# Optimization experiments

Hardware: AMD Instinct MI355X
Metric: run time of the kernel (lower is better)

Reference implementation:

```python
import jax, jax.numpy as jnp
import numpy as np

B, Q, E = 32768, 1024, 1024  # batch, quant_dim, embed_dim


def setup_inputs() -> dict:
    key = jax.random.key(0)
    k1, k2, k3, k4, k5 = jax.random.split(key, 5)
    s = lambda n: 1.0 / np.sqrt(n)
    x = jax.random.normal(k1, (B, Q), jnp.float32)
    # nn.Linear weights, shape [out_features, in_features]
    W1 = jax.random.normal(k2, (2 * Q, Q), jnp.float32) * s(Q)      # selector layer 1
    W2 = jax.random.normal(k3, (Q, 2 * Q), jnp.float32) * s(2 * Q)  # selector layer 2
    W3 = jax.random.normal(k4, (Q, Q), jnp.float32) * s(Q)          # selector layer 3
    Wc = jax.random.normal(k5, (E, Q), jnp.float32) * s(Q)          # codebook
    return {"x": x, "W1": W1, "W2": W2, "W3": W3, "Wc": Wc}


def dyn_k_hot(x, k_scores):
    # k per row = argmax(k_scores) + 1
    k_values = jnp.argmax(k_scores, axis=-1, keepdims=True) + 1  # [B,1]
    # torch: sorted_indices = argsort(x, descending); mask gathered by argsort(sorted_indices)
    # equivalently: rank of each element in descending order < k
    ranks = jnp.argsort(jnp.argsort(-x, axis=-1), axis=-1)       # [B,Q]
    return (ranks < k_values).astype(x.dtype)


def reference(x, W1, W2, W3, Wc):
    # dynkselector: Linear -> ReLU -> Linear -> ReLU -> Linear (no biases)
    h = jax.nn.relu(x @ W1.T)
    h = jax.nn.relu(h @ W2.T)
    k_scores = h @ W3.T
    k_hot = dyn_k_hot(x, k_scores)   # [B,Q] {0,1}
    return k_hot @ Wc.T              # codebook projection -> [B,E]
```

## Files before the change

### kernel.cpp

```cpp
#include <hip/hip_runtime.h>
#include <stdint.h>

#define B_  32768
#define Q_  1024
#define E_  1024
#define CAPF  16384
#define CAPF2 1024

typedef __attribute__((ext_vector_type(8))) short bf16x8;
typedef __attribute__((ext_vector_type(8))) _Float16 f16x8;
typedef __attribute__((ext_vector_type(8))) unsigned short u16x8;
typedef __attribute__((ext_vector_type(4))) float f32x4;
typedef unsigned short us;

__device__ __forceinline__ f32x4 MFMA16(bf16x8 a, bf16x8 b, f32x4 c) {
    return __builtin_amdgcn_mfma_f32_16x16x32_bf16(a, b, c, 0, 0, 0);
}
__device__ __forceinline__ f32x4 MFMA16H(bf16x8 a, bf16x8 b, f32x4 c) {
    return __builtin_amdgcn_mfma_f32_16x16x32_f16(
        __builtin_bit_cast(f16x8, a), __builtin_bit_cast(f16x8, b), c, 0, 0, 0);
}

__device__ __forceinline__ us f2bf(float v) {
    unsigned u = __float_as_uint(v);
    u += 0x7FFFu + ((u >> 16) & 1u);
    return (us)(u >> 16);
}
__device__ __forceinline__ float bf2f(us b) {
    return __uint_as_float(((unsigned)b) << 16);
}
__device__ __forceinline__ us f2h(float v) {
    _Float16 h = (_Float16)v;
    return __builtin_bit_cast(unsigned short, h);
}

__global__ __launch_bounds__(256)
void split_planes_k(const float* __restrict__ in, us* __restrict__ hi,
                    us* __restrict__ lo, int n8) {
    int i = blockIdx.x * 256 + threadIdx.x;
    const int stride = gridDim.x * 256;
    for (; i < n8; i += stride) {
        float4 a = ((const float4*)in)[i * 2];
        float4 b = ((const float4*)in)[i * 2 + 1];
        float f[8] = {a.x, a.y, a.z, a.w, b.x, b.y, b.z, b.w};
        u16x8 h, l;
#pragma unroll
        for (int j = 0; j < 8; ++j) {
            us c0 = f2bf(f[j]);
            h[j] = c0;
            l[j] = f2bf(f[j] - bf2f(c0));
        }
        ((u16x8*)hi)[i] = h;
        ((u16x8*)lo)[i] = l;
    }
}

__global__ __launch_bounds__(256)
void cvt_plane_k(const float* __restrict__ in, us* __restrict__ hi, int n8) {
    int i = blockIdx.x * 256 + threadIdx.x;
    const int stride = gridDim.x * 256;
    for (; i < n8; i += stride) {
        float4 a = ((const float4*)in)[i * 2];
        float4 b = ((const float4*)in)[i * 2 + 1];
        float f[8] = {a.x, a.y, a.z, a.w, b.x, b.y, b.z, b.w};
        u16x8 h;
#pragma unroll
        for (int j = 0; j < 8; ++j) h[j] = f2bf(f[j]);
        ((u16x8*)hi)[i] = h;
    }
}

__global__ __launch_bounds__(256)
void cvt_plane_h(const float* __restrict__ in, us* __restrict__ hi, int n8) {
    int i = blockIdx.x * 256 + threadIdx.x;
    const int stride = gridDim.x * 256;
    for (; i < n8; i += stride) {
        float4 a = ((const float4*)in)[i * 2];
        float4 b = ((const float4*)in)[i * 2 + 1];
        float f[8] = {a.x, a.y, a.z, a.w, b.x, b.y, b.z, b.w};
        u16x8 h;
#pragma unroll
        for (int j = 0; j < 8; ++j) h[j] = f2h(f[j]);
        ((u16x8*)hi)[i] = h;
    }
}

__global__ __launch_bounds__(256)
void gather_split(const float* __restrict__ X, const int* __restrict__ flags,
                  const int* __restrict__ cnt, us* __restrict__ G0,
                  us* __restrict__ G1) {
    const int n = min(*cnt, CAPF);
    for (int it = blockIdx.x; it < n; it += gridDim.x) {
        int row = flags[it];
        if ((unsigned)row >= B_) row = 0;
        float4 v = ((const float4*)(X + (size_t)row * Q_))[threadIdx.x];
        float f[4] = {v.x, v.y, v.z, v.w};
        us h[4], l[4];
#pragma unroll
        for (int j = 0; j < 4; ++j) {
            h[j] = f2bf(f[j]);
            l[j] = f2bf(f[j] - bf2f(h[j]));
        }
        *(uint2*)&G0[(size_t)it * Q_ + threadIdx.x * 4] = *(uint2*)h;
        *(uint2*)&G1[(size_t)it * Q_ + threadIdx.x * 4] = *(uint2*)l;
    }
}

#define LGKM0() asm volatile("s_waitcnt lgkmcnt(0)" ::: "memory")
#define VMC8()  asm volatile("s_waitcnt vmcnt(8)" ::: "memory")
#define BAR()   __builtin_amdgcn_s_barrier()
#define RD_AB(Aarr, Barr, slot) { \
    const us* _la = &LA[(slot) * 8192]; const us* _lb = &LB[(slot) * 8192]; \
    _Pragma("unroll") for (int mf = 0; mf < 8; ++mf) Aarr[mf] = *(const bf16x8*)&_la[ago[mf]]; \
    _Pragma("unroll") for (int nf = 0; nf < 4; ++nf) Barr[nf] = *(const bf16x8*)&_lb[bgo[nf]]; }
#define CLX(AF, BF) { __builtin_amdgcn_s_setprio(1); \
    _Pragma("unroll") for (int mf = 0; mf < 8; ++mf) { \
        _Pragma("unroll") for (int nf = 0; nf < 4; ++nf) { \
            if constexpr (FP16) acc[mf][nf] = MFMA16H(AF[mf], BF[nf], acc[mf][nf]); \
            else               acc[mf][nf] = MFMA16 (AF[mf], BF[nf], acc[mf][nf]); } } \
    __builtin_amdgcn_s_setprio(0); }

template<int NSEG, int K, int EMIT, bool RELU, bool FP16>
__global__ __launch_bounds__(512, 2)
void gemm4r(const us* __restrict__ A0p, const us* __restrict__ A1p,
            const us* __restrict__ B0p, const us* __restrict__ B1p,
            void* __restrict__ Cp0, void* __restrict__ Cp1, int N) {
    constexpr int TPS = K / 32;
    constexpr int NT  = NSEG * TPS;
    static_assert(NT % 2 == 0 && NT >= 4, "shape");
    __shared__ __align__(16) us LA[4 * 8192];
    __shared__ __align__(16) us LB[4 * 8192];

    const int t = threadIdx.x;
    const int wv = t >> 6, lane = t & 63;
    const int lanelo = lane & 15, kq = lane >> 4;
    const int wm = wv >> 2, wn = wv & 3;

    const int q8 = gridDim.x >> 3;
    const int logical = ((int)blockIdx.x & 7) * q8 + ((int)blockIdx.x >> 3);
    const int gx = N >> 8;
    const int m0 = (logical / gx) * 256, n0 = (logical % gx) * 256;

    int soff[2], ldst[2];
#pragma unroll
    for (int i = 0; i < 2; ++i) {
        int s = i * 512 + t;
        int row = s >> 2, c = s & 3;
        soff[i] = row * K + (c ^ ((row >> 1) & 3)) * 8;
        ldst[i] = (i * 512 + wv * 64) * 8;
    }
    int ago[8], bgo[4];
#pragma unroll
    for (int mf = 0; mf < 8; ++mf) {
        int row = wm * 128 + mf * 16 + lanelo;
        ago[mf] = (row * 4 + (kq ^ ((row >> 1) & 3))) * 8;
    }
#pragma unroll
    for (int nf = 0; nf < 4; ++nf) {
        int row = wn * 64 + nf * 16 + lanelo;
        bgo[nf] = (row * 4 + (kq ^ ((row >> 1) & 3))) * 8;
    }

    auto stage = [&](int tv) {
        int slot = tv & 3;
        int seg = tv / TPS;
        int kb  = (tv - seg * TPS) * 32;
        const us* Ap = (NSEG == 1 || seg < 2) ? A0p : A1p;
        const us* Bp = (NSEG == 3 && seg == 1) ? B1p : B0p;
        const us* Abase = Ap + (size_t)m0 * K + kb;
        const us* Bbase = Bp + (size_t)n0 * K + kb;
        us* dA = &LA[slot * 8192];
        us* dB = &LB[slot * 8192];
#pragma unroll
        for (int i = 0; i < 2; ++i) {
            __builtin_amdgcn_global_load_lds(
                (const __attribute__((address_space(1))) void*)(Abase + soff[i]),
                (__attribute__((address_space(3))) void*)(dA + ldst[i]), 16, 0, 0);
            __builtin_amdgcn_global_load_lds(
                (const __attribute__((address_space(1))) void*)(Bbase + soff[i]),
                (__attribute__((address_space(3))) void*)(dB + ldst[i]), 16, 0, 0);
        }
    };

    f32x4 acc[8][4];
#pragma unroll
    for (int i = 0; i < 8; ++i)
#pragma unroll
        for (int j = 0; j < 4; ++j) acc[i][j] = (f32x4){0.f, 0.f, 0.f, 0.f};

    bf16x8 aE[8], bE[4], aO[8], bO[4];

    stage(0); stage(1); stage(2);
    VMC8();  BAR();
    RD_AB(aE, bE, 0);
    stage(3);
    LGKM0(); VMC8(); BAR();

    for (int tt = 0; tt < NT; tt += 2) {
        RD_AB(aO, bO, (tt + 1) & 3);
        { int tv = tt + 4; if (tv > NT - 1) tv = NT - 1; stage(tv); }
        CLX(aE, bE);
        LGKM0(); VMC8(); BAR();
        { int tn = (tt + 2 < NT) ? (tt + 2) : (NT - 1);
          RD_AB(aE, bE, tn & 3); }
        { int tv = tt + 5; if (tv > NT - 1) tv = NT - 1; stage(tv); }
        CLX(aO, bO);
        LGKM0(); VMC8(); BAR();
    }

#pragma unroll
    for (int mf = 0; mf < 8; ++mf)
#pragma unroll
        for (int nf = 0; nf < 4; ++nf)
#pragma unroll
            for (int r = 0; r < 4; ++r) {
                int row = m0 + wm * 128 + mf * 16 + kq * 4 + r;
                int col = n0 + wn * 64 + nf * 16 + lanelo;
                float v = acc[mf][nf][r];
                if constexpr (RELU) v = fmaxf(v, 0.f);
                if constexpr (EMIT == 1) {
                    us c0 = f2bf(v);
                    ((us*)Cp0)[(size_t)row * N + col] = c0;
                    ((us*)Cp1)[(size_t)row * N + col] = f2bf(v - bf2f(c0));
                } else if constexpr (EMIT == 2) {
                    ((us*)Cp0)[(size_t)row * N + col] = f2h(v);
                } else {
                    ((float*)Cp0)[(size_t)row * N + col] = v;
                }
            }
}

template<int NPASS, bool RELU, bool EMITP, bool DYN>
__global__ __launch_bounds__(256, 4)
void gemm_pp(const us* __restrict__ A0, const us* __restrict__ A1,
             const us* __restrict__ B0, const us* __restrict__ B1,
             void* __restrict__ Cp0, void* __restrict__ Cp1,
             int N, int K, const int* __restrict__ ncnt) {
    __shared__ __align__(16) us A0s[128 * 32];
    __shared__ __align__(16) us B0s[128 * 32];
    __shared__ __align__(16) us A1s[(NPASS == 3) ? 128 * 32 : 8];
    __shared__ __align__(16) us B1s[(NPASS == 3) ? 128 * 32 : 8];

    const int t = threadIdx.x;
    const int wave = t >> 6, lane = t & 63;
    const int lanelo = lane & 15, kq = lane >> 4;
    const int wm = wave >> 1, wn = wave & 1;
    const int q8 = gridDim.x >> 3;
    const int logical = ((int)blockIdx.x & 7) * q8 + ((int)blockIdx.x >> 3);
    const int gx = N >> 7;
    const int m0 = (logical / gx) * 128, n0 = (logical % gx) * 128;

    if constexpr (DYN) {
        int nn = *ncnt; if (nn > CAPF) nn = CAPF;
        if (m0 >= ((nn + 127) & ~127)) return;
    }

    f32x4 acc[4][4];
#pragma unroll
    for (int i = 0; i < 4; ++i)
#pragma unroll
        for (int j = 0; j < 4; ++j) acc[i][j] = (f32x4){0.f, 0.f, 0.f, 0.f};

    for (int kt = 0; kt < K; kt += 32) {
        __syncthreads();
#pragma unroll
        for (int g = 0; g < 2; ++g) {
            int c = (g * 4 + wave) * 64 + lane;
            int row = c >> 2;
            int koff = (c & 3) ^ (row & 3);
            size_t offa = (size_t)(m0 + row) * K + kt + koff * 8;
            size_t offb = (size_t)(n0 + row) * K + kt + koff * 8;
            int dst = (g * 4 + wave) * 512;
            __builtin_amdgcn_global_load_lds(
                (const __attribute__((address_space(1))) void*)(A0 + offa),
                (__attribute__((address_space(3))) void*)&A0s[dst], 16, 0, 0);
            __builtin_amdgcn_global_load_lds(
                (const __attribute__((address_space(1))) void*)(B0 + offb),
                (__attribute__((address_space(3))) void*)&B0s[dst], 16, 0, 0);
            if constexpr (NPASS == 3) {
                __builtin_amdgcn_global_load_lds(
                    (const __attribute__((address_space(1))) void*)(A1 + offa),
                    (__attribute__((address_space(3))) void*)&A1s[dst], 16, 0, 0);
                __builtin_amdgcn_global_load_lds(
                    (const __attribute__((address_space(1))) void*)(B1 + offb),
                    (__attribute__((address_space(3))) void*)&B1s[dst], 16, 0, 0);
            }
        }
        __syncthreads();

        bf16x8 a0[4], a1[4];
#pragma unroll
        for (int mf = 0; mf < 4; ++mf) {
            int ar = wm * 64 + mf * 16 + lanelo;
            int ac = ar * 4 + (kq ^ (ar & 3));
            a0[mf] = *(const bf16x8*)&A0s[ac * 8];
            if constexpr (NPASS == 3) a1[mf] = *(const bf16x8*)&A1s[ac * 8];
        }
#pragma unroll
        for (int nf = 0; nf < 4; ++nf) {
            int br = wn * 64 + nf * 16 + lanelo;
            int bc = br * 4 + (kq ^ (br & 3));
            bf16x8 vb0 = *(const bf16x8*)&B0s[bc * 8];
#pragma unroll
            for (int mf = 0; mf < 4; ++mf) acc[mf][nf] = MFMA16(a0[mf], vb0, acc[mf][nf]);
            if constexpr (NPASS == 3) {
                bf16x8 vb1 = *(const bf16x8*)&B1s[bc * 8];
#pragma unroll
                for (int mf = 0; mf < 4; ++mf) acc[mf][nf] = MFMA16(a0[mf], vb1, acc[mf][nf]);
#pragma unroll
                for (int mf = 0; mf < 4; ++mf) acc[mf][nf] = MFMA16(a1[mf], vb0, acc[mf][nf]);
            }
        }
    }

#pragma unroll
    for (int mf = 0; mf < 4; ++mf)
#pragma unroll
        for (int nf = 0; nf < 4; ++nf)
#pragma unroll
            for (int r = 0; r < 4; ++r) {
                int row = m0 + wm * 64 + mf * 16 + kq * 4 + r;
                int col = n0 + wn * 64 + nf * 16 + lanelo;
                float v = acc[mf][nf][r];
                if constexpr (RELU) v = fmaxf(v, 0.f);
                if constexpr (EMITP) {
                    us c0 = f2bf(v);
                    ((us*)Cp0)[(size_t)row * N + col] = c0;
                    ((us*)Cp1)[(size_t)row * N + col] = f2bf(v - bf2f(c0));
                } else {
                    ((float*)Cp0)[(size_t)row * N + col] = v;
                }
            }
}

__device__ __forceinline__ int chunk_of(int row, int koff) {
    return row * 4 + (koff ^ (row & 3));
}

template<int NPASS>
__device__ __forceinline__ void split_store(us* S0, us* S1,
                                            int rowX, int koffX, float4 a, float4 b) {
    int ch = chunk_of(rowX, koffX);
    float f[8] = {a.x, a.y, a.z, a.w, b.x, b.y, b.z, b.w};
    bf16x8 lo, hi;
#pragma unroll
    for (int j = 0; j < 8; ++j) {
        us c0 = f2bf(f[j]);
        lo[j] = (short)c0;
        hi[j] = (short)f2bf(f[j] - bf2f(c0));
    }
    *(bf16x8*)&S0[ch * 8] = lo;
    if constexpr (NPASS == 3) *(bf16x8*)&S1[ch * 8] = hi;
}

template<int NPASS, bool AF32, bool RELU, bool EMITP>
__global__ __launch_bounds__(256, 2)
void gemm3p(const void* __restrict__ Ap0, const void* __restrict__ Ap1,
            const float* __restrict__ Wf,
            void* __restrict__ Cp0, void* __restrict__ Cp1,
            int M, int N, int K) {
    __shared__ __align__(16) us A0s[128 * 32];
    __shared__ __align__(16) us B0s[128 * 32];
    __shared__ __align__(16) us A1s[(NPASS == 3) ? 128 * 32 : 8];
    __shared__ __align__(16) us B1s[(NPASS == 3) ? 128 * 32 : 8];

    const int t = threadIdx.x;
    const int wave = t >> 6, lane = t & 63;
    const int lanelo = lane & 15, kq = lane >> 4;
    const int wm = wave >> 1, wn = wave & 1;
    const int m0 = blockIdx.y * 128, n0 = blockIdx.x * 128;
    const int brow = t >> 1, bhalf = t & 1;

    f32x4 acc[4][4];
#pragma unroll
    for (int i = 0; i < 4; ++i)
#pragma unroll
        for (int j = 0; j < 4; ++j) acc[i][j] = (f32x4){0.f, 0.f, 0.f, 0.f};

    for (int kt = 0; kt < K; kt += 32) {
        __syncthreads();
        const float* wp = Wf + (size_t)(n0 + brow) * K + kt + bhalf * 16;
        float4 v0 = *(const float4*)(wp + 0);
        float4 v1 = *(const float4*)(wp + 4);
        float4 v2 = *(const float4*)(wp + 8);
        float4 v3 = *(const float4*)(wp + 12);
        if constexpr (AF32) {
            const float* ap = (const float*)Ap0 + (size_t)(m0 + brow) * K + kt + bhalf * 16;
            float4 u0 = *(const float4*)(ap + 0);
            float4 u1 = *(const float4*)(ap + 4);
            float4 u2 = *(const float4*)(ap + 8);
            float4 u3 = *(const float4*)(ap + 12);
            split_store<NPASS>(A0s, A1s, brow, bhalf * 2 + 0, u0, u1);
            split_store<NPASS>(A0s, A1s, brow, bhalf * 2 + 1, u2, u3);
        } else {
#pragma unroll
            for (int g = 0; g < 2; ++g) {
                int c = (g * 4 + wave) * 64 + lane;
                int row = c >> 2;
                int koff = (c & 3) ^ (row & 3);
                const us* s0 = (const us*)Ap0 + (size_t)(m0 + row) * K + kt + koff * 8;
                __builtin_amdgcn_global_load_lds(
                    (const __attribute__((address_space(1))) void*)s0,
                    (__attribute__((address_space(3))) void*)&A0s[(size_t)(g * 4 + wave) * 512],
                    16, 0, 0);
                if constexpr (NPASS == 3) {
                    const us* s1 = (const us*)Ap1 + (size_t)(m0 + row) * K + kt + koff * 8;
                    __builtin_amdgcn_global_load_lds(
                        (const __attribute__((address_space(1))) void*)s1,
                        (__attribute__((address_space(3))) void*)&A1s[(size_t)(g * 4 + wave) * 512],
                        16, 0, 0);
                }
            }
        }
        split_store<NPASS>(B0s, B1s, brow, bhalf * 2 + 0, v0, v1);
        split_store<NPASS>(B0s, B1s, brow, bhalf * 2 + 1, v2, v3);
        __syncthreads();

        bf16x8 a0[4], a1[4];
#pragma unroll
        for (int mf = 0; mf < 4; ++mf) {
            int ar = wm * 64 + mf * 16 + lanelo;
            int ac = chunk_of(ar, kq);
            a0[mf] = *(const bf16x8*)&A0s[ac * 8];
            if constexpr (NPASS == 3) a1[mf] = *(const bf16x8*)&A1s[ac * 8];
        }
#pragma unroll
        for (int nf = 0; nf < 4; ++nf) {
            int br = wn * 64 + nf * 16 + lanelo;
            int bc = chunk_of(br, kq);
            bf16x8 vb0 = *(const bf16x8*)&B0s[bc * 8];
#pragma unroll
            for (int mf = 0; mf < 4; ++mf) acc[mf][nf] = MFMA16(a0[mf], vb0, acc[mf][nf]);
            if constexpr (NPASS == 3) {
                bf16x8 vb1 = *(const bf16x8*)&B1s[bc * 8];
#pragma unroll
                for (int mf = 0; mf < 4; ++mf) acc[mf][nf] = MFMA16(a0[mf], vb1, acc[mf][nf]);
#pragma unroll
                for (int mf = 0; mf < 4; ++mf) acc[mf][nf] = MFMA16(a1[mf], vb0, acc[mf][nf]);
            }
        }
    }

#pragma unroll
    for (int mf = 0; mf < 4; ++mf)
#pragma unroll
        for (int nf = 0; nf < 4; ++nf)
#pragma unroll
            for (int r = 0; r < 4; ++r) {
                int row = m0 + wm * 64 + mf * 16 + kq * 4 + r;
                int col = n0 + wn * 64 + nf * 16 + lanelo;
                float v = acc[mf][nf][r];
                if constexpr (RELU) v = fmaxf(v, 0.f);
                if constexpr (EMITP) {
                    us c0 = f2bf(v);
                    ((us*)Cp0)[(size_t)row * N + col] = c0;
                    ((us*)Cp1)[(size_t)row * N + col] = f2bf(v - bf2f(c0));
                } else {
                    ((float*)Cp0)[(size_t)row * N + col] = v;
                }
            }
}

__global__ __launch_bounds__(256)
void row_argmax_flag(const float* __restrict__ S, int* __restrict__ KV,
                     int* __restrict__ flags, int* __restrict__ cnt, float theta) {
    int row = blockIdx.x * 4 + (threadIdx.x >> 6);
    int lane = threadIdx.x & 63;
    const float* s = S + (size_t)row * Q_;
    float b1 = -3.4e38f, b2 = -3.4e38f; int i1 = 0;
    for (int j = lane; j < Q_; j += 64) {
        float v = s[j];
        if (v > b1) { b2 = b1; b1 = v; i1 = j; }
        else if (v > b2) b2 = v;
    }
#pragma unroll
    for (int m = 1; m < 64; m <<= 1) {
        float o1 = __shfl_xor(b1, m);
        int   oi = __shfl_xor(i1, m);
        float o2 = __shfl_xor(b2, m);
        if (o1 > b1 || (o1 == b1 && oi < i1)) {
            b2 = fmaxf(b1, o2);
            b1 = o1; i1 = oi;
        } else {
            b2 = fmaxf(b2, o1);
        }
    }
    if (lane == 0) {
        KV[row] = i1 + 1;
        if (b1 - b2 < theta) {
            int p = atomicAdd(cnt, 1);
            if (p < CAPF) flags[p] = row;
        }
    }
}

__global__ __launch_bounds__(256)
void g_argmax_flag2(const float* __restrict__ SCg, const int* __restrict__ flags,
                    const int* __restrict__ cnt, int* __restrict__ KV,
                    int* __restrict__ flags2, int* __restrict__ cnt2) {
    const int lane = threadIdx.x & 63, wv = threadIdx.x >> 6;
    const int n = min(*cnt, CAPF);
    for (int it = blockIdx.x * 4 + wv; it < n; it += gridDim.x * 4) {
        const float* s = SCg + (size_t)it * Q_;
        float b1 = -3.4e38f, b2 = -3.4e38f; int i1 = 0;
        for (int j = lane; j < Q_; j += 64) {
            float v = s[j];
            if (v > b1) { b2 = b1; b1 = v; i1 = j; }
            else if (v > b2) b2 = v;
        }
#pragma unroll
        for (int m = 1; m < 64; m <<= 1) {
            float o1 = __shfl_xor(b1, m);
            int   oi = __shfl_xor(i1, m);
            float o2 = __shfl_xor(b2, m);
            if (o1 > b1 || (o1 == b1 && oi < i1)) {
                b2 = fmaxf(b1, o2);
                b1 = o1; i1 = oi;
            } else {
                b2 = fmaxf(b2, o1);
            }
        }
        if (lane == 0) {
            int r = flags[it];
            if ((unsigned)r < B_) {
                KV[r] = i1 + 1;
                if (b1 - b2 < 1e-3f) {
                    int p = atomicAdd(cnt2, 1);
                    if (p < CAPF2) flags2[p] = r;
                }
            }
        }
    }
}

template<int K, bool IN_BY_FLAG, bool RELU>
__global__ __launch_bounds__(256)
void rescore_gemm(const float* __restrict__ IN, const float* __restrict__ W,
                  float* __restrict__ OUT, const int* __restrict__ flags,
                  const int* __restrict__ cnt, int N, int cap) {
    __shared__ float xr[K];
    const int t = threadIdx.x, lane = t & 63, wv = t >> 6;
    const int n = min(*cnt, cap);
    const int chunks = N >> 4;
    for (int w = blockIdx.x; w < n * chunks; w += gridDim.x) {
        const int it = w / chunks, ch = w - it * chunks;
        int srow = IN_BY_FLAG ? flags[it] : it;
        if (IN_BY_FLAG && (unsigned)srow >= B_) srow = 0;
        const float* rp = IN + (size_t)srow * K;
        __syncthreads();
#pragma unroll
        for (int p = t; p < K / 4; p += 256)
            ((float4*)xr)[p] = ((const float4*)rp)[p];
        __syncthreads();
#pragma unroll
        for (int jj = 0; jj < 4; ++jj) {
            const int col = ch * 16 + wv * 4 + jj;
            const float* wr = W + (size_t)col * K;
            double a0 = 0.0, a1 = 0.0;
#pragma unroll
            for (int i = 0; i < K / 256; ++i) {
                const int k = i * 256 + lane * 4;
                float4 w4 = *(const float4*)(wr + k);
                float4 x4 = *(const float4*)(xr + k);
                a0 += (double)x4.x * w4.x + (double)x4.y * w4.y;
                a1 += (double)x4.z * w4.z + (double)x4.w * w4.w;
            }
            double a = a0 + a1;
#pragma unroll
            for (int m = 1; m < 64; m <<= 1) a += __shfl_xor(a, m);
            if (lane == 0) {
                float v = (float)a;
                if (RELU) v = fmaxf(v, 0.f);
                OUT[(size_t)it * N + col] = v;
            }
        }
    }
}

__global__ __launch_bounds__(256)
void rescore_argmax(const float* __restrict__ SCF, const int* __restrict__ flags,
                    const int* __restrict__ cnt, int* __restrict__ KV, int cap) {
    const int lane = threadIdx.x & 63, wv = threadIdx.x >> 6;
    const int n = min(*cnt, cap);
    for (int it = blockIdx.x * 4 + wv; it < n; it += gridDim.x * 4) {
        const float* s = SCF + (size_t)it * Q_;
        float best = -3.4e38f; int bi = 0;
        for (int j = lane; j < Q_; j += 64) {
            float v = s[j];
            if (v > best) { best = v; bi = j; }
        }
#pragma unroll
        for (int m = 1; m < 64; m <<= 1) {
            float ov = __shfl_xor(best, m); int oi = __shfl_xor(bi, m);
            if (ov > best || (ov == best && oi < bi)) { best = ov; bi = oi; }
        }
        if (lane == 0) {
            int r = flags[it];
            if ((unsigned)r < B_) KV[r] = bi + 1;
        }
    }
}

__global__ __launch_bounds__(256)
void topk_mask_radix(const float* __restrict__ X, const int* __restrict__ KV,
                     us* __restrict__ Mout) {
    const int row  = blockIdx.x * 4 + (threadIdx.x >> 6);
    const int lane = threadIdx.x & 63;
    const float* x = X + (size_t)row * Q_;

    unsigned u[16];
#pragma unroll
    for (int j4 = 0; j4 < 4; ++j4) {
        float4 v = *(const float4*)(x + lane * 16 + j4 * 4);
        float f[4] = {v.x, v.y, v.z, v.w};
#pragma unroll
        for (int e = 0; e < 4; ++e) {
            unsigned fb = __float_as_uint(f[e]);
            u[j4 * 4 + e] = (fb & 0x80000000u) ? ~fb : (fb | 0x80000000u);
        }
    }
    const int k = KV[row];

    unsigned p = 0;
#pragma unroll
    for (int b = 31; b >= 0; --b) {
        unsigned q = p | (1u << b);
        int c = 0;
#pragma unroll
        for (int j = 0; j < 16; ++j) c += (u[j] >= q);
#pragma unroll
        for (int m = 1; m < 64; m <<= 1) c += __shfl_xor(c, m);
        if (c >= k) p = q;
    }

    int gt = 0, eqloc = 0;
#pragma unroll
    for (int j = 0; j < 16; ++j) { gt += (u[j] > p); eqloc += (u[j] == p); }
    int gtot = gt;
#pragma unroll
    for (int m = 1; m < 64; m <<= 1) gtot += __shfl_xor(gtot, m);
    int scan = eqloc;
#pragma unroll
    for (int d = 1; d < 64; d <<= 1) {
        int o = __shfl_up(scan, d);
        if (lane >= d) scan += o;
    }
    int run = scan - eqloc;
    const int quota = k - gtot;

    us m16[16];
#pragma unroll
    for (int j = 0; j < 16; ++j) {
        bool one;
        if (u[j] > p) one = true;
        else if (u[j] == p) { one = (run < quota); ++run; }
        else one = false;
        m16[j] = one ? (us)0x3F80 : (us)0;
    }
    u16x8* dst = (u16x8*)(Mout + (size_t)row * Q_ + lane * 16);
    dst[0] = *(u16x8*)&m16[0];
    dst[1] = *(u16x8*)&m16[8];
}

extern "C" void kernel_launch(void* const* d_in, const int* in_sizes, int n_in,
                              void* d_out, int out_size, void* d_ws, size_t ws_size,
                              hipStream_t stream) {
    const float* x  = (const float*)d_in[0];
    const float* W1 = (const float*)d_in[1];
    const float* W2 = (const float*)d_in[2];
    const float* W3 = (const float*)d_in[3];
    const float* Wc = (const float*)d_in[4];
    float* out = (float*)d_out;

    char* ws = (char*)d_ws;
    char* dob = (char*)d_out;
    us*    H1f  = (us*)ws;
    float* SC   = (float*)(ws + ((size_t)128 << 20));
    us*    H1g0 = (us*)ws;
    us*    H1g1 = (us*)(ws + ((size_t)64 << 20));
    float* SCg  = (float*)(ws + ((size_t)128 << 20));
    us*    MASKB= (us*)(ws + ((size_t)192 << 20));
    int* KV     = (int*)(ws + ((size_t)256 << 20));
    int* FLAGS  = KV + B_;
    int* CNT    = FLAGS + B_;
    int* CNT2   = CNT + 1;
    int* FLAGS2 = CNT2 + 1;
    us*    Xf   = (us*)dob;
    us*    H2f  = (us*)(dob + ((size_t)64 << 20));
    us*    Xg0  = (us*)dob;
    us*    Xg1  = (us*)(dob + ((size_t)32 << 20));
    us*    H2g0 = (us*)(dob + ((size_t)64 << 20));
    us*    H2g1 = (us*)(dob + ((size_t)96 << 20));
    float* H1F  = (float*)dob;
    float* H2F  = (float*)(dob + ((size_t)8 << 20));
    float* SCF  = (float*)(dob + ((size_t)12 << 20));
    char* WP = ws + ((size_t)256 << 20) + ((size_t)512 << 10);
    us* W1h = (us*)WP;                       us* W1f = (us*)WP;
    us* W1l = W1h + (size_t)2 * Q_ * Q_;
    us* W2h = W1l + (size_t)2 * Q_ * Q_;     us* W2f = W1l;
    us* W2l = W2h + (size_t)2 * Q_ * Q_;
    us* W3h = W2l + (size_t)2 * Q_ * Q_;     us* W3f = W2h;
    us* W3l = W3h + (size_t)Q_ * Q_;
    us* Wch = W3l + (size_t)Q_ * Q_;
    const size_t NEEDED = ((size_t)256 << 20) + ((size_t)512 << 10) + ((size_t)22 << 20);

    hipMemsetAsync(CNT, 0, 2 * sizeof(int), stream);
    dim3 blk(256);

    if (ws_size >= NEEDED) {
        cvt_plane_h<<<dim3(2048), blk, 0, stream>>>(x,  Xf,  B_ * Q_ / 8);
        cvt_plane_h<<<dim3(512),  blk, 0, stream>>>(W1, W1f, 2 * Q_ * Q_ / 8);
        cvt_plane_h<<<dim3(512),  blk, 0, stream>>>(W2, W2f, 2 * Q_ * Q_ / 8);
        cvt_plane_h<<<dim3(512),  blk, 0, stream>>>(W3, W3f, Q_ * Q_ / 8);
        gemm4r<1, Q_,     2, true,  true ><<<dim3(1024), dim3(512), 0, stream>>>(
            Xf,  nullptr, W1f, nullptr, H1f, nullptr, 2 * Q_);
        gemm4r<1, 2 * Q_, 2, true,  true ><<<dim3(512),  dim3(512), 0, stream>>>(
            H1f, nullptr, W2f, nullptr, H2f, nullptr, Q_);
        gemm4r<1, Q_,     0, false, true ><<<dim3(512),  dim3(512), 0, stream>>>(
            H2f, nullptr, W3f, nullptr, SC,  nullptr, Q_);
        row_argmax_flag<<<dim3(B_ / 4), blk, 0, stream>>>(SC, KV, FLAGS, CNT, 0.01f);
        split_planes_k<<<dim3(512), blk, 0, stream>>>(W1, W1h, W1l, 2 * Q_ * Q_ / 8);
        split_planes_k<<<dim3(512), blk, 0, stream>>>(W2, W2h, W2l, 2 * Q_ * Q_ / 8);
        split_planes_k<<<dim3(512), blk, 0, stream>>>(W3, W3h, W3l, Q_ * Q_ / 8);
        cvt_plane_k   <<<dim3(512), blk, 0, stream>>>(Wc, Wch, E_ * Q_ / 8);
        gather_split<<<dim3(2048), blk, 0, stream>>>(x, FLAGS, CNT, Xg0, Xg1);
        gemm_pp<3, true,  true,  true><<<dim3((CAPF / 128) * (2 * Q_ / 128)), blk, 0, stream>>>(
            Xg0,  Xg1,  W1h, W1l, H1g0, H1g1, 2 * Q_, Q_, CNT);
        gemm_pp<3, true,  true,  true><<<dim3((CAPF / 128) * (Q_ / 128)), blk, 0, stream>>>(
            H1g0, H1g1, W2h, W2l, H2g0, H2g1, Q_, 2 * Q_, CNT);
        gemm_pp<3, false, false, true><<<dim3((CAPF / 128) * (Q_ / 128)), blk, 0, stream>>>(
            H2g0, H2g1, W3h, W3l, SCg, nullptr, Q_, Q_, CNT);
        g_argmax_flag2<<<dim3(1024), blk, 0, stream>>>(SCg, FLAGS, CNT, KV, FLAGS2, CNT2);
        rescore_gemm<Q_,     true,  true ><<<dim3(4096), blk, 0, stream>>>(x,   W1, H1F, FLAGS2, CNT2, 2 * Q_, CAPF2);
        rescore_gemm<2 * Q_, false, true ><<<dim3(2048), blk, 0, stream>>>(H1F, W2, H2F, FLAGS2, CNT2, Q_,     CAPF2);
        rescore_gemm<Q_,     false, false><<<dim3(2048), blk, 0, stream>>>(H2F, W3, SCF, FLAGS2, CNT2, Q_,     CAPF2);
        rescore_argmax<<<dim3(64), blk, 0, stream>>>(SCF, FLAGS2, CNT2, KV, CAPF2);
        topk_mask_radix<<<dim3(B_ / 4), blk, 0, stream>>>(x, KV, MASKB);
        gemm4r<1, Q_, 0, false, false><<<dim3(512), dim3(512), 0, stream>>>(
            MASKB, nullptr, Wch, nullptr, out, nullptr, E_);
    } else {
        us*    H1_0 = (us*)ws;
        us*    H1_1 = (us*)(ws + ((size_t)128 << 20));
        float* SCo  = (float*)ws;
        us*    MB   = (us*)(ws + ((size_t)128 << 20));
        us* H2_0 = (us*)d_out;
        us* H2_1 = (us*)d_out + (size_t)B_ * Q_;
        float* H1Fo = (float*)ws;
        float* H2Fo = (float*)(ws + ((size_t)128 << 20));
        float* SCFo = (float*)(ws + ((size_t)192 << 20));
        gemm3p<3, true,  true,  true ><<<dim3(2 * Q_ / 128, B_ / 128), blk, 0, stream>>>(
            x, nullptr, W1, H1_0, H1_1, B_, 2 * Q_, Q_);
        gemm3p<3, false, true,  true ><<<dim3(Q_ / 128, B_ / 128), blk, 0, stream>>>(
            H1_0, H1_1, W2, H2_0, H2_1, B_, Q_, 2 * Q_);
        gemm3p<3, false, false, false><<<dim3(Q_ / 128, B_ / 128), blk, 0, stream>>>(
            H2_0, H2_1, W3, SCo, nullptr, B_, Q_, Q_);
        row_argmax_flag<<<dim3(B_ / 4), blk, 0, stream>>>(SCo, KV, FLAGS, CNT, 1e-3f);
        rescore_gemm<Q_,     true,  true ><<<dim3(4096), blk, 0, stream>>>(x,    W1, H1Fo, FLAGS, CNT, 2 * Q_, CAPF);
        rescore_gemm<2 * Q_, false, true ><<<dim3(2048), blk, 0, stream>>>(H1Fo, W2, H2Fo, FLAGS, CNT, Q_,     CAPF);
        rescore_gemm<Q_,     false, false><<<dim3(2048), blk, 0, stream>>>(H2Fo, W3, SCFo, FLAGS, CNT, Q_,     CAPF);
        rescore_argmax<<<dim3(64), blk, 0, stream>>>(SCFo, FLAGS, CNT, KV, CAPF);
        topk_mask_radix<<<dim3(B_ / 4), blk, 0, stream>>>(x, KV, MB);
        gemm3p<1, false, false, false><<<dim3(E_ / 128, B_ / 128), blk, 0, stream>>>(
            MB, nullptr, Wc, out, nullptr, B_, E_, Q_);
    }
}
```

Baseline: 1.298 ms.

## Split-K the refinement GEMMs with fp32 partials and a finalize reduction kernel

Replaces the three-pass refinement GEMM with a split-K variant. The grid gets a second dimension of 4 K-splits, and the three bf16 product passes run sequentially through one LDS buffer pair, so each tile loads only two operands per step. Each split writes fp32 partials, and a separate finalize kernel sums them and applies ReLU and the hi/lo split. It also lowers the flagged-row capacity from 16384 to 4096 and changes the LDS swizzle pattern. The aim is more parallelism for small flagged counts, at the cost of extra partial-sum memory traffic and more launches. The lower cap risks silently dropping flagged rows if more than 4096 are flagged.

```diff
diff --git a/kernel.cpp b/kernel.cpp
--- a/kernel.cpp
+++ b/kernel.cpp
@@ -4,7 +4,7 @@
 #define B_  32768
 #define Q_  1024
 #define E_  1024
-#define CAPF  16384
+#define CAPF  4096
 #define CAPF2 1024
 
 typedef __attribute__((ext_vector_type(8))) short bf16x8;
@@ -103,6 +103,39 @@
         }
         *(uint2*)&G0[(size_t)it * Q_ + threadIdx.x * 4] = *(uint2*)h;
         *(uint2*)&G1[(size_t)it * Q_ + threadIdx.x * 4] = *(uint2*)l;
+    }
+}
+
+template<int SPLITS, int MODE>
+__global__ __launch_bounds__(256)
+void finalize_k(const float* __restrict__ P, size_t pstride,
+                us* __restrict__ o0, us* __restrict__ o1,
+                float* __restrict__ of, const int* __restrict__ cnt, int N) {
+    const int n = min(*cnt, CAPF);
+    const int total4 = n * (N >> 2);
+    int i = blockIdx.x * 256 + threadIdx.x;
+    const int stride = gridDim.x * 256;
+    for (; i < total4; i += stride) {
+        float4 s = ((const float4*)P)[i];
+#pragma unroll
+        for (int sp = 1; sp < SPLITS; ++sp) {
+            float4 p = *(const float4*)(P + (size_t)sp * pstride + (size_t)i * 4);
+            s.x += p.x; s.y += p.y; s.z += p.z; s.w += p.w;
+        }
+        if constexpr (MODE == 0) {
+            ((float4*)of)[i] = s;
+        } else {
+            float f[4] = {fmaxf(s.x, 0.f), fmaxf(s.y, 0.f),
+                          fmaxf(s.z, 0.f), fmaxf(s.w, 0.f)};
+            us h[4], l[4];
+#pragma unroll
+            for (int j = 0; j < 4; ++j) {
+                h[j] = f2bf(f[j]);
+                l[j] = f2bf(f[j] - bf2f(h[j]));
+            }
+            *(uint2*)&o0[(size_t)i * 4] = *(uint2*)h;
+            *(uint2*)&o1[(size_t)i * 4] = *(uint2*)l;
+        }
     }
 }
 
@@ -230,11 +263,11 @@
             }
 }
 
-template<int NPASS, bool RELU, bool EMITP, bool DYN>
+template<int NPASS, int SPLITS>
 __global__ __launch_bounds__(256, 4)
-void gemm_pp(const us* __restrict__ A0, const us* __restrict__ A1,
+void gemm_sp(const us* __restrict__ A0, const us* __restrict__ A1,
              const us* __restrict__ B0, const us* __restrict__ B1,
-             void* __restrict__ Cp0, void* __restrict__ Cp1,
+             float* __restrict__ P, size_t pstride,
              int N, int K, const int* __restrict__ ncnt) {
     __shared__ __align__(16) us A0s[128 * 32];
     __shared__ __align__(16) us B0s[128 * 32];
@@ -249,11 +282,14 @@
     const int logical = ((int)blockIdx.x & 7) * q8 + ((int)blockIdx.x >> 3);
     const int gx = N >> 7;
     const int m0 = (logical / gx) * 128, n0 = (logical % gx) * 128;
-
-    if constexpr (DYN) {
-        int nn = *ncnt; if (nn > CAPF) nn = CAPF;
-        if (m0 >= ((nn + 127) & ~127)) return;
-    }
+    const int split = blockIdx.y;
+
+    int nn = *ncnt; if (nn > CAPF) nn = CAPF;
+    if (m0 >= ((nn + 127) & ~127)) return;
+
+    const int Ks = K / SPLITS;
+    const int kbase = split * Ks;
+    const int tps = Ks >> 5;
 
     f32x4 acc[4][4];
 #pragma unroll
@@ -261,58 +297,47 @@
 #pragma unroll
         for (int j = 0; j < 4; ++j) acc[i][j] = (f32x4){0.f, 0.f, 0.f, 0.f};
 
-    for (int kt = 0; kt < K; kt += 32) {
+    for (int vt = 0; vt < NPASS * tps; ++vt) {
+        const int seg = vt / tps;
+        const int kt  = kbase + (vt - seg * tps) * 32;
+        const us* Ap = (NPASS == 1 || seg < 2) ? A0 : A1;
+        const us* Bp = (NPASS == 3 && seg == 1) ? B1 : B0;
         __syncthreads();
 #pragma unroll
         for (int g = 0; g < 2; ++g) {
             int c = (g * 4 + wave) * 64 + lane;
             int row = c >> 2;
-            int koff = (c & 3) ^ (row & 3);
+            int koff = (c & 3) ^ ((row >> 1) & 3);
             size_t offa = (size_t)(m0 + row) * K + kt + koff * 8;
             size_t offb = (size_t)(n0 + row) * K + kt + koff * 8;
             int dst = (g * 4 + wave) * 512;
             __builtin_amdgcn_global_load_lds(
-                (const __attribute__((address_space(1))) void*)(A0 + offa),
+                (const __attribute__((address_space(1))) void*)(Ap + offa),
                 (__attribute__((address_space(3))) void*)&A0s[dst], 16, 0, 0);
             __builtin_amdgcn_global_load_lds(
-                (const __attribute__((address_space(1))) void*)(B0 + offb),
+                (const __attribute__((address_space(1))) void*)(Bp + offb),
                 (__attribute__((address_space(3))) void*)&B0s[dst], 16, 0, 0);
-            if constexpr (NPASS == 3) {
-                __builtin_amdgcn_global_load_lds(
-                    (const __attribute__((address_space(1))) void*)(A1 + offa),
-                    (__attribute__((address_space(3))) void*)&A1s[dst], 16, 0, 0);
-                __builtin_amdgcn_global_load_lds(
-                    (const __attribute__((address_space(1))) void*)(B1 + offb),
-                    (__attribute__((address_space(3))) void*)&B1s[dst], 16, 0, 0);
-            }
         }
         __syncthreads();
 
-        bf16x8 a0[4], a1[4];
+        bf16x8 a0[4];
 #pragma unroll
         for (int mf = 0; mf < 4; ++mf) {
             int ar = wm * 64 + mf * 16 + lanelo;
-            int ac = ar * 4 + (kq ^ (ar & 3));
+            int ac = ar * 4 + (kq ^ ((ar >> 1) & 3));
             a0[mf] = *(const bf16x8*)&A0s[ac * 8];
-            if constexpr (NPASS == 3) a1[mf] = *(const bf16x8*)&A1s[ac * 8];
         }
 #pragma unroll
         for (int nf = 0; nf < 4; ++nf) {
             int br = wn * 64 + nf * 16 + lanelo;
-            int bc = br * 4 + (kq ^ (br & 3));
+            int bc = br * 4 + (kq ^ ((br >> 1) & 3));
             bf16x8 vb0 = *(const bf16x8*)&B0s[bc * 8];
 #pragma unroll
             for (int mf = 0; mf < 4; ++mf) acc[mf][nf] = MFMA16(a0[mf], vb0, acc[mf][nf]);
-            if constexpr (NPASS == 3) {
-                bf16x8 vb1 = *(const bf16x8*)&B1s[bc * 8];
-#pragma unroll
-                for (int mf = 0; mf < 4; ++mf) acc[mf][nf] = MFMA16(a0[mf], vb1, acc[mf][nf]);
-#pragma unroll
-                for (int mf = 0; mf < 4; ++mf) acc[mf][nf] = MFMA16(a1[mf], vb0, acc[mf][nf]);
-            }
-        }
-    }
-
+        }
+    }
+
+    float* Pd = P + (size_t)split * pstride;
 #pragma unroll
     for (int mf = 0; mf < 4; ++mf)
 #pragma unroll
@@ -321,15 +346,7 @@
             for (int r = 0; r < 4; ++r) {
                 int row = m0 + wm * 64 + mf * 16 + kq * 4 + r;
                 int col = n0 + wn * 64 + nf * 16 + lanelo;
-                float v = acc[mf][nf][r];
-                if constexpr (RELU) v = fmaxf(v, 0.f);
-                if constexpr (EMITP) {
-                    us c0 = f2bf(v);
-                    ((us*)Cp0)[(size_t)row * N + col] = c0;
-                    ((us*)Cp1)[(size_t)row * N + col] = f2bf(v - bf2f(c0));
-                } else {
-                    ((float*)Cp0)[(size_t)row * N + col] = v;
-                }
+                Pd[(size_t)row * N + col] = acc[mf][nf][r];
             }
 }
 
@@ -676,9 +693,12 @@
     char* dob = (char*)d_out;
     us*    H1f  = (us*)ws;
     float* SC   = (float*)(ws + ((size_t)128 << 20));
-    us*    H1g0 = (us*)ws;
-    us*    H1g1 = (us*)(ws + ((size_t)64 << 20));
-    float* SCg  = (float*)(ws + ((size_t)128 << 20));
+    float* P1   = (float*)ws;
+    us*    H1g0 = (us*)(ws + ((size_t)128 << 20));
+    us*    H1g1 = (us*)(ws + ((size_t)144 << 20));
+    us*    H2g0 = (us*)(ws + ((size_t)160 << 20));
+    us*    H2g1 = (us*)(ws + ((size_t)168 << 20));
+    float* SCg  = (float*)(ws + ((size_t)176 << 20));
     us*    MASKB= (us*)(ws + ((size_t)192 << 20));
     int* KV     = (int*)(ws + ((size_t)256 << 20));
     int* FLAGS  = KV + B_;
@@ -689,8 +709,7 @@
     us*    H2f  = (us*)(dob + ((size_t)64 << 20));
     us*    Xg0  = (us*)dob;
     us*    Xg1  = (us*)(dob + ((size_t)32 << 20));
-    us*    H2g0 = (us*)(dob + ((size_t)64 << 20));
-    us*    H2g1 = (us*)(dob + ((size_t)96 << 20));
+    float* P23  = (float*)(dob + ((size_t)64 << 20));
     float* H1F  = (float*)dob;
     float* H2F  = (float*)(dob + ((size_t)8 << 20));
     float* SCF  = (float*)(dob + ((size_t)12 << 20));
@@ -703,6 +722,9 @@
     us* W3l = W3h + (size_t)Q_ * Q_;
     us* Wch = W3l + (size_t)Q_ * Q_;
     const size_t NEEDED = ((size_t)256 << 20) + ((size_t)512 << 10) + ((size_t)22 << 20);
+
+    const size_t PS1 = (size_t)CAPF * 2 * Q_;
+    const size_t PS2 = (size_t)CAPF * Q_;
 
     hipMemsetAsync(CNT, 0, 2 * sizeof(int), stream);
     dim3 blk(256);
@@ -724,12 +746,15 @@
         split_planes_k<<<dim3(512), blk, 0, stream>>>(W3, W3h, W3l, Q_ * Q_ / 8);
         cvt_plane_k   <<<dim3(512), blk, 0, stream>>>(Wc, Wch, E_ * Q_ / 8);
         gather_split<<<dim3(2048), blk, 0, stream>>>(x, FLAGS, CNT, Xg0, Xg1);
-        gemm_pp<3, true,  true,  true><<<dim3((CAPF / 128) * (2 * Q_ / 128)), blk, 0, stream>>>(
-            Xg0,  Xg1,  W1h, W1l, H1g0, H1g1, 2 * Q_, Q_, CNT);
-        gemm_pp<3, true,  true,  true><<<dim3((CAPF / 128) * (Q_ / 128)), blk, 0, stream>>>(
-            H1g0, H1g1, W2h, W2l, H2g0, H2g1, Q_, 2 * Q_, CNT);
-        gemm_pp<3, false, false, true><<<dim3((CAPF / 128) * (Q_ / 128)), blk, 0, stream>>>(
-            H2g0, H2g1, W3h, W3l, SCg, nullptr, Q_, Q_, CNT);
+        gemm_sp<3, 4><<<dim3((CAPF / 128) * (2 * Q_ / 128), 4), blk, 0, stream>>>(
+            Xg0,  Xg1,  W1h, W1l, P1,  PS1, 2 * Q_, Q_, CNT);
+        finalize_k<4, 1><<<dim3(2048), blk, 0, stream>>>(P1,  PS1, H1g0, H1g1, nullptr, CNT, 2 * Q_);
+        gemm_sp<3, 4><<<dim3((CAPF / 128) * (Q_ / 128), 4), blk, 0, stream>>>(
+            H1g0, H1g1, W2h, W2l, P23, PS2, Q_, 2 * Q_, CNT);
+        finalize_k<4, 1><<<dim3(2048), blk, 0, stream>>>(P23, PS2, H2g0, H2g1, nullptr, CNT, Q_);
+        gemm_sp<3, 4><<<dim3((CAPF / 128) * (Q_ / 128), 4), blk, 0, stream>>>(
+            H2g0, H2g1, W3h, W3l, P23, PS2, Q_, Q_, CNT);
+        finalize_k<4, 0><<<dim3(2048), blk, 0, stream>>>(P23, PS2, nullptr, nullptr, SCg, CNT, Q_);
         g_argmax_flag2<<<dim3(1024), blk, 0, stream>>>(SCg, FLAGS, CNT, KV, FLAGS2, CNT2);
         rescore_gemm<Q_,     true,  true ><<<dim3(4096), blk, 0, stream>>>(x,   W1, H1F, FLAGS2, CNT2, 2 * Q_, CAPF2);
         rescore_gemm<2 * Q_, false, true ><<<dim3(2048), blk, 0, stream>>>(H1F, W2, H2F, FLAGS2, CNT2, Q_,     CAPF2);
```

Result: faster. 1.080 ms (-16.8%).
